# Kernel optimization log

Measured on AMD Instinct MI355X. Metric: run time of the kernel, lower is better.

## Reference

```python
import jax, jax.numpy as jnp
import numpy as np

RADIUS = 8.0   # matches init kwarg radius
EPS = 1e-8     # nn.CosineSimilarity eps


def _denorm(p, height, width):
    # kornia denormalize_pixel_coordinates: [-1,1] -> [0, size-1]
    scale = jnp.array([(width - 1) * 0.5, (height - 1) * 0.5], dtype=p.dtype)
    return (p + 1.0) * scale


def setup_inputs() -> dict:
    key = jax.random.key(0)
    k1, k2, k3, k4 = jax.random.split(key, 4)
    B, N, D = 4, 2048, 256
    features = jax.random.normal(k1, (B, N, D), dtype=jnp.float32)
    pts_src = jax.random.uniform(k2, (B, N, 2), dtype=jnp.float32) * 2.0 - 1.0
    pts_dst = jax.random.uniform(k3, (B, B, N, 2), dtype=jnp.float32) * 2.0 - 1.0
    invis_idx = jax.random.randint(k4, (3, 128), 0, N)
    return {"features": features, "pts_src": pts_src, "pts_dst": pts_dst,
            "invis_idx": invis_idx, "height": 480, "width": 640}


def reference(features, pts_src, pts_dst, invis_idx, height, width):
    # features: [B,N,D]; pts_src: [B,N,2]; pts_dst: [B,B,N,2]
    B, N, D = features.shape
    ps = _denorm(jax.lax.stop_gradient(pts_src), height, width)   # [B,N,2]
    pd = _denorm(jax.lax.stop_gradient(pts_dst), height, width)   # [B,B,N,2]

    # squared euclidean distance d2[i,j,n,m] = ||ps[i,n] - pd[i,j,m]||^2
    s_src = jnp.sum(ps * ps, axis=-1)          # [B,N]
    s_dst = jnp.sum(pd * pd, axis=-1)          # [B,B,N]
    cross = jnp.einsum('ind,ijmd->ijnm', ps, pd)
    d2 = s_src[:, None, :, None] + s_dst[:, :, None, :] - 2.0 * cross  # [B,B,N,N]
    mask = d2 <= RADIUS * RADIUS

    # pair p = i*B + j of the flattened [B^2] grid matches src batch j (p % B)
    # with dst batch i (p // B):
    # cos[i,j,n,m] = <features[j,n], features[i,m]> / max(|f_jn|*|f_im|, eps)
    dots = jnp.einsum('jnd,imd->ijnm', features, features)  # [B,B,N,N]
    norms = jnp.sqrt(jnp.sum(features * features, axis=-1))  # [B,N]
    denom = jnp.maximum(norms[None, :, :, None] * norms[:, None, None, :], EPS)
    cos = dots / denom

    cnt = jnp.maximum(jnp.sum(mask), 1).astype(features.dtype)
    return jnp.sum(jnp.where(mask, 1.0 - cos, 0.0)) / cnt
```

## Files before the change

### kernel.cpp

```cpp
#include <hip/hip_runtime.h>

#define BB 4
#define NN 2048
#define DD 256
#define TILE_N 32
#define NPW 8
#define NT (NN / TILE_N)
#define MLEN NN
#define MCH (MLEN / 128)
#define WQ_CAP 128
#define NBLK (BB * BB * NT)

__global__ __launch_bounds__(256, 4) void scan_kernel(const float* __restrict__ feat,
                                                      const float* __restrict__ pts_src,
                                                      const float* __restrict__ pts_dst,
                                                      const int* __restrict__ hptr,
                                                      const int* __restrict__ wptr,
                                                      float* __restrict__ psum,
                                                      unsigned int* __restrict__ pcnt) {
    __shared__ unsigned int wq[4][WQ_CAP];
    __shared__ unsigned int wqc[4];
    __shared__ float bsum[4];
    __shared__ unsigned int bcnt[4];

    const int xcd  = blockIdx.x & 7;
    const int slot = blockIdx.x >> 3;
    const int pair = xcd | ((slot >> 6) << 3);
    const int tile = slot & 63;
    const int i = pair >> 2;
    const int j = pair & 3;
    const float sx = ((float)(*wptr) - 1.0f) * 0.5f;
    const float sy = ((float)(*hptr) - 1.0f) * 0.5f;

    const int wave = threadIdx.x >> 6;
    const int lane = threadIdx.x & 63;
    if (lane == 0) wqc[wave] = 0u;

    const int nbase = tile * TILE_N + wave * NPW;
    float psx[NPW], psy[NPW];
#pragma unroll
    for (int k = 0; k < NPW; ++k) {
        psx[k] = fmaf(pts_src[(size_t)(i * NN + nbase + k) * 2 + 0], sx, sx);
        psy[k] = fmaf(pts_src[(size_t)(i * NN + nbase + k) * 2 + 1], sy, sy);
    }

    const float4* pd = (const float4*)(pts_dst + (size_t)pair * NN * 2);

    float4 q = pd[lane];
#pragma unroll 4
    for (int c = 0; c < MCH; ++c) {
        float4 qn;
        if (c + 1 < MCH) qn = pd[(c + 1) * 64 + lane];
        const float qx0 = fmaf(q.x, sx, sx), qy0 = fmaf(q.y, sy, sy);
        const float qx1 = fmaf(q.z, sx, sx), qy1 = fmaf(q.w, sy, sy);
        float mn = 1e30f;
#pragma unroll
        for (int k = 0; k < NPW; ++k) {
            const float ax = psx[k] - qx0, ay = psy[k] - qy0;
            const float bx = psx[k] - qx1, by = psy[k] - qy1;
            mn = fminf(mn, fminf(fmaf(ax, ax, ay * ay), fmaf(bx, bx, by * by)));
        }
        if (__ballot(mn <= 64.0f)) {
            const unsigned int m2 = (unsigned int)(c * 128 + 2 * lane);
#pragma unroll
            for (int k = 0; k < NPW; ++k) {
                const float ax = psx[k] - qx0, ay = psy[k] - qy0;
                const float bx = psx[k] - qx1, by = psy[k] - qy1;
                const float d0 = fmaf(ax, ax, ay * ay);
                const float d1 = fmaf(bx, bx, by * by);
                if (fminf(d0, d1) <= 64.0f) {
                    if (d0 <= 64.0f) {
                        const unsigned int slot2 = atomicAdd(&wqc[wave], 1u);
                        if (slot2 < WQ_CAP) wq[wave][slot2] = ((unsigned int)k << 11) | m2;
                    }
                    if (d1 <= 64.0f) {
                        const unsigned int slot2 = atomicAdd(&wqc[wave], 1u);
                        if (slot2 < WQ_CAP) wq[wave][slot2] = ((unsigned int)k << 11) | (m2 + 1u);
                    }
                }
            }
        }
        q = qn;
    }

    const unsigned int hc = min(wqc[wave], (unsigned int)WQ_CAP);
    const int g = lane >> 3, sub = lane & 7;
    float lsum = 0.0f;
    for (unsigned int h0 = 0; h0 < hc; h0 += 8) {
        const unsigned int hid = h0 + (unsigned int)g;
        const bool valid = hid < hc;
        float dd = 0.0f, aa = 0.0f, bb = 0.0f;
        if (valid) {
            const unsigned int rec = wq[wave][hid];
            const int m = (int)(rec & 2047u);
            const int n = nbase + (int)(rec >> 11);
            const float4* pa = (const float4*)(feat + (size_t)(j * NN + n) * DD);
            const float4* pb = (const float4*)(feat + (size_t)(i * NN + m) * DD);
#pragma unroll
            for (int t = 0; t < 8; ++t) {
                const float4 a = pa[t * 8 + sub];
                const float4 b = pb[t * 8 + sub];
                dd = fmaf(a.x, b.x, fmaf(a.y, b.y, fmaf(a.z, b.z, fmaf(a.w, b.w, dd))));
                aa = fmaf(a.x, a.x, fmaf(a.y, a.y, fmaf(a.z, a.z, fmaf(a.w, a.w, aa))));
                bb = fmaf(b.x, b.x, fmaf(b.y, b.y, fmaf(b.z, b.z, fmaf(b.w, b.w, bb))));
            }
        }
        dd += __shfl_xor(dd, 1, 64);  aa += __shfl_xor(aa, 1, 64);  bb += __shfl_xor(bb, 1, 64);
        dd += __shfl_xor(dd, 2, 64);  aa += __shfl_xor(aa, 2, 64);  bb += __shfl_xor(bb, 2, 64);
        dd += __shfl_xor(dd, 4, 64);  aa += __shfl_xor(aa, 4, 64);  bb += __shfl_xor(bb, 4, 64);
        if (valid && sub == 0) {
            const float p = aa * bb;
            float r = rsqrtf(p);
            r = r * (1.5f - 0.5f * p * r * r);
            lsum += 1.0f - dd * r;
        }
    }
#pragma unroll
    for (int off = 32; off >= 1; off >>= 1) lsum += __shfl_xor(lsum, off, 64);

    if (lane == 0) { bsum[wave] = lsum; bcnt[wave] = hc; }
    __syncthreads();
    if (threadIdx.x == 0) {
        psum[blockIdx.x] = bsum[0] + bsum[1] + bsum[2] + bsum[3];
        pcnt[blockIdx.x] = bcnt[0] + bcnt[1] + bcnt[2] + bcnt[3];
    }
}

__global__ __launch_bounds__(256) void finalize_kernel(const float* __restrict__ psum,
                                                       const unsigned int* __restrict__ pcnt,
                                                       float* __restrict__ out) {
    float s = 0.0f;
    float c = 0.0f;
    for (int t = threadIdx.x; t < NBLK; t += 256) {
        s += psum[t];
        c += (float)pcnt[t];
    }
#pragma unroll
    for (int off = 32; off >= 1; off >>= 1) {
        s += __shfl_xor(s, off, 64);
        c += __shfl_xor(c, off, 64);
    }
    __shared__ float ss[4], cc[4];
    const int wave = threadIdx.x >> 6;
    const int lane = threadIdx.x & 63;
    if (lane == 0) { ss[wave] = s; cc[wave] = c; }
    __syncthreads();
    if (threadIdx.x == 0) {
        const float S = ss[0] + ss[1] + ss[2] + ss[3];
        const float C = cc[0] + cc[1] + cc[2] + cc[3];
        out[0] = S / fmaxf(C, 1.0f);
    }
}

extern "C" void kernel_launch(void* const* d_in, const int* in_sizes, int n_in,
                              void* d_out, int out_size, void* d_ws, size_t ws_size,
                              hipStream_t stream) {
    const float* feat    = (const float*)d_in[0];
    const float* pts_src = (const float*)d_in[1];
    const float* pts_dst = (const float*)d_in[2];
    const int* hptr = (const int*)d_in[4];
    const int* wptr = (const int*)d_in[5];
    float* out = (float*)d_out;

    float*        psum  = (float*)d_ws;
    unsigned int* pcnt  = (unsigned int*)((char*)d_ws + 8192);

    scan_kernel<<<NBLK, 256, 0, stream>>>(feat, pts_src, pts_dst,
                                          hptr, wptr, psum, pcnt);
    finalize_kernel<<<1, 256, 0, stream>>>(psum, pcnt, out);
}
```

Baseline: 88.71 us.

## Fuse finalize into scan kernel via keyed per-block records and spin-wait

Removes the separate finalize kernel launch. Each block publishes its partial sum and count together with two block-specific key words using release stores. Block 0 spin-waits with acquire loads until every record shows its keys, then reduces and writes the output. This saves one kernel launch and its gap, but block 0 stays resident and busy-waits, and if it were scheduled before the others could run this could deadlock. The keys only guard against stale workspace contents by chance, since the workspace is never cleared between calls.

```diff
diff --git a/kernel.cpp b/kernel.cpp
--- a/kernel.cpp
+++ b/kernel.cpp
@@ -11,17 +11,21 @@
 #define WQ_CAP 128
 #define NBLK (BB * BB * NT)
 
+#define KEY1 0xA5C3E7D1u
+#define KEY2 0x3B9ACA07u
+
 __global__ __launch_bounds__(256, 4) void scan_kernel(const float* __restrict__ feat,
                                                       const float* __restrict__ pts_src,
                                                       const float* __restrict__ pts_dst,
                                                       const int* __restrict__ hptr,
                                                       const int* __restrict__ wptr,
-                                                      float* __restrict__ psum,
-                                                      unsigned int* __restrict__ pcnt) {
+                                                      unsigned int* __restrict__ recs,
+                                                      float* __restrict__ out) {
     __shared__ unsigned int wq[4][WQ_CAP];
     __shared__ unsigned int wqc[4];
     __shared__ float bsum[4];
     __shared__ unsigned int bcnt[4];
+    __shared__ float rsum[4], rcnt[4];
 
     const int xcd  = blockIdx.x & 7;
     const int slot = blockIdx.x >> 3;
@@ -70,12 +74,12 @@
                 const float d1 = fmaf(bx, bx, by * by);
                 if (fminf(d0, d1) <= 64.0f) {
                     if (d0 <= 64.0f) {
-                        const unsigned int slot2 = atomicAdd(&wqc[wave], 1u);
-                        if (slot2 < WQ_CAP) wq[wave][slot2] = ((unsigned int)k << 11) | m2;
+                        const unsigned int s2 = atomicAdd(&wqc[wave], 1u);
+                        if (s2 < WQ_CAP) wq[wave][s2] = ((unsigned int)k << 11) | m2;
                     }
                     if (d1 <= 64.0f) {
-                        const unsigned int slot2 = atomicAdd(&wqc[wave], 1u);
-                        if (slot2 < WQ_CAP) wq[wave][slot2] = ((unsigned int)k << 11) | (m2 + 1u);
+                        const unsigned int s2 = atomicAdd(&wqc[wave], 1u);
+                        if (s2 < WQ_CAP) wq[wave][s2] = ((unsigned int)k << 11) | (m2 + 1u);
                     }
                 }
             }
@@ -121,33 +125,39 @@
     if (lane == 0) { bsum[wave] = lsum; bcnt[wave] = hc; }
     __syncthreads();
     if (threadIdx.x == 0) {
-        psum[blockIdx.x] = bsum[0] + bsum[1] + bsum[2] + bsum[3];
-        pcnt[blockIdx.x] = bcnt[0] + bcnt[1] + bcnt[2] + bcnt[3];
+        const float S = bsum[0] + bsum[1] + bsum[2] + bsum[3];
+        const unsigned int C = bcnt[0] + bcnt[1] + bcnt[2] + bcnt[3];
+        unsigned int* rec = recs + 4u * blockIdx.x;
+        __hip_atomic_store(rec + 0, __float_as_uint(S), __ATOMIC_RELAXED, __HIP_MEMORY_SCOPE_AGENT);
+        __hip_atomic_store(rec + 1, C,                  __ATOMIC_RELAXED, __HIP_MEMORY_SCOPE_AGENT);
+        __hip_atomic_store(rec + 2, KEY1 ^ blockIdx.x,  __ATOMIC_RELEASE, __HIP_MEMORY_SCOPE_AGENT);
+        __hip_atomic_store(rec + 3, KEY2 ^ blockIdx.x,  __ATOMIC_RELEASE, __HIP_MEMORY_SCOPE_AGENT);
     }
-}
+    if (blockIdx.x != 0) return;
 
-__global__ __launch_bounds__(256) void finalize_kernel(const float* __restrict__ psum,
-                                                       const unsigned int* __restrict__ pcnt,
-                                                       float* __restrict__ out) {
-    float s = 0.0f;
-    float c = 0.0f;
+    float s = 0.0f, c = 0.0f;
     for (int t = threadIdx.x; t < NBLK; t += 256) {
-        s += psum[t];
-        c += (float)pcnt[t];
+        unsigned int* rec = recs + 4u * (unsigned int)t;
+        const unsigned int e1 = KEY1 ^ (unsigned int)t;
+        const unsigned int e2 = KEY2 ^ (unsigned int)t;
+        while (__hip_atomic_load(rec + 2, __ATOMIC_ACQUIRE, __HIP_MEMORY_SCOPE_AGENT) != e1 ||
+               __hip_atomic_load(rec + 3, __ATOMIC_ACQUIRE, __HIP_MEMORY_SCOPE_AGENT) != e2) {
+            __builtin_amdgcn_s_sleep(8);
+        }
+        s += __uint_as_float(__hip_atomic_load(rec + 0, __ATOMIC_RELAXED, __HIP_MEMORY_SCOPE_AGENT));
+        c += (float)__hip_atomic_load(rec + 1, __ATOMIC_RELAXED, __HIP_MEMORY_SCOPE_AGENT);
     }
 #pragma unroll
     for (int off = 32; off >= 1; off >>= 1) {
         s += __shfl_xor(s, off, 64);
         c += __shfl_xor(c, off, 64);
     }
-    __shared__ float ss[4], cc[4];
-    const int wave = threadIdx.x >> 6;
-    const int lane = threadIdx.x & 63;
-    if (lane == 0) { ss[wave] = s; cc[wave] = c; }
+    __syncthreads();
+    if (lane == 0) { rsum[wave] = s; rcnt[wave] = c; }
     __syncthreads();
     if (threadIdx.x == 0) {
-        const float S = ss[0] + ss[1] + ss[2] + ss[3];
-        const float C = cc[0] + cc[1] + cc[2] + cc[3];
+        const float S = rsum[0] + rsum[1] + rsum[2] + rsum[3];
+        const float C = rcnt[0] + rcnt[1] + rcnt[2] + rcnt[3];
         out[0] = S / fmaxf(C, 1.0f);
     }
 }
@@ -162,10 +172,8 @@
     const int* wptr = (const int*)d_in[5];
     float* out = (float*)d_out;
 
-    float*        psum  = (float*)d_ws;
-    unsigned int* pcnt  = (unsigned int*)((char*)d_ws + 8192);
+    unsigned int* recs = (unsigned int*)d_ws;
 
     scan_kernel<<<NBLK, 256, 0, stream>>>(feat, pts_src, pts_dst,
-                                          hptr, wptr, psum, pcnt);
-    finalize_kernel<<<1, 256, 0, stream>>>(psum, pcnt, out);
+                                          hptr, wptr, recs, out);
 }
```

Measured after the change: 110.9 us. +25.0%, slower.

## Replace brute-force radius scan with uniform spatial grid binning of dst points

Applied to the files above, without the earlier changes.

Adds a build kernel that buckets each pair's destination points into a 40x30 grid of 16-pixel cells using a counting sort with a shared prefix scan. The match kernel then checks only the 3x3 neighbouring cells for each source point, split across 8 column octants per tile, in place of scanning all 2048 dst points. This removes the O(N^2) distance work but adds an extra launch, serial per-thread loops of uneven length, and a gather through the permutation array. Each wave's hit queue is capped at 160 entries for 64 source points, so dense neighbourhoods could overflow and be silently dropped.

```diff
diff --git a/kernel.cpp b/kernel.cpp
--- a/kernel.cpp
+++ b/kernel.cpp
@@ -3,21 +3,103 @@
 #define BB 4
 #define NN 2048
 #define DD 256
-#define TILE_N 32
-#define NPW 8
-#define NT (NN / TILE_N)
-#define MLEN NN
-#define MCH (MLEN / 128)
-#define WQ_CAP 128
-#define NBLK (BB * BB * NT)
-
-__global__ __launch_bounds__(256, 4) void scan_kernel(const float* __restrict__ feat,
-                                                      const float* __restrict__ pts_src,
-                                                      const float* __restrict__ pts_dst,
-                                                      const int* __restrict__ hptr,
-                                                      const int* __restrict__ wptr,
-                                                      float* __restrict__ psum,
-                                                      unsigned int* __restrict__ pcnt) {
+#define GCX 40
+#define GCY 30
+#define NCELL (GCX * GCY)
+#define CSTRIDE 1216
+#define OCTW 5
+#define STILE 256
+#define NTIL (NN / STILE)
+#define MBLK (BB * BB * NTIL * 8)
+#define WQ_CAP 160
+
+#define OFF_BX    131072
+#define OFF_BM    (131072 + 262144)
+#define OFF_PSUM  (131072 + 262144 + 131072)
+#define OFF_PCNT  (OFF_PSUM + 4096)
+
+__device__ __forceinline__ int cell_clamp(int v, int hi) {
+    return v < 0 ? 0 : (v > hi ? hi : v);
+}
+
+__global__ __launch_bounds__(256) void build_kernel(const float* __restrict__ pts_dst,
+                                                    const int* __restrict__ hptr,
+                                                    const int* __restrict__ wptr,
+                                                    int* __restrict__ starts,
+                                                    float2* __restrict__ bx,
+                                                    int* __restrict__ bm) {
+    __shared__ int cnt[NCELL];
+    __shared__ int tsum[256];
+    const int pair = blockIdx.x;
+    const float sx = ((float)(*wptr) - 1.0f) * 0.5f;
+    const float sy = ((float)(*hptr) - 1.0f) * 0.5f;
+
+    for (int t = threadIdx.x; t < NCELL; t += 256) cnt[t] = 0;
+    __syncthreads();
+
+    const float2* pd = (const float2*)(pts_dst + (size_t)pair * NN * 2);
+    float qx[8], qy[8]; int qc[8];
+#pragma unroll
+    for (int k = 0; k < 8; ++k) {
+        const float2 r = pd[threadIdx.x + k * 256];
+        qx[k] = fmaf(r.x, sx, sx);
+        qy[k] = fmaf(r.y, sy, sy);
+        const int cx = cell_clamp((int)(qx[k] * 0.0625f), GCX - 1);
+        const int cy = cell_clamp((int)(qy[k] * 0.0625f), GCY - 1);
+        qc[k] = cx + GCX * cy;
+        atomicAdd(&cnt[qc[k]], 1);
+    }
+    __syncthreads();
+
+    const int base = threadIdx.x * 5;
+    int loc[5]; int s = 0;
+#pragma unroll
+    for (int k = 0; k < 5; ++k) {
+        const int c = base + k;
+        const int v = (c < NCELL) ? cnt[c] : 0;
+        loc[k] = s; s += v;
+    }
+    tsum[threadIdx.x] = s;
+    __syncthreads();
+    for (int off = 1; off < 256; off <<= 1) {
+        const int v = (threadIdx.x >= off) ? tsum[threadIdx.x - off] : 0;
+        __syncthreads();
+        tsum[threadIdx.x] += v;
+        __syncthreads();
+    }
+    const int tbase = tsum[threadIdx.x] - s;
+    int* gst = starts + pair * CSTRIDE;
+#pragma unroll
+    for (int k = 0; k < 5; ++k) {
+        const int c = base + k;
+        if (c < NCELL) {
+            const int st = tbase + loc[k];
+            gst[c] = st;
+            cnt[c] = st;
+        }
+    }
+    if (threadIdx.x == 0) gst[NCELL] = NN;
+    __syncthreads();
+
+    float2* gbx = bx + (size_t)pair * NN;
+    int*    gbm = bm + (size_t)pair * NN;
+#pragma unroll
+    for (int k = 0; k < 8; ++k) {
+        const int pos = atomicAdd(&cnt[qc[k]], 1);
+        gbx[pos] = make_float2(qx[k], qy[k]);
+        gbm[pos] = threadIdx.x + k * 256;
+    }
+}
+
+__global__ __launch_bounds__(256, 4) void match_kernel(const float* __restrict__ feat,
+                                                       const float* __restrict__ pts_src,
+                                                       const int* __restrict__ hptr,
+                                                       const int* __restrict__ wptr,
+                                                       const int* __restrict__ starts,
+                                                       const float2* __restrict__ bx,
+                                                       const int* __restrict__ bm,
+                                                       float* __restrict__ psum,
+                                                       unsigned int* __restrict__ pcnt) {
     __shared__ unsigned int wq[4][WQ_CAP];
     __shared__ unsigned int wqc[4];
     __shared__ float bsum[4];
@@ -25,8 +107,10 @@
 
     const int xcd  = blockIdx.x & 7;
     const int slot = blockIdx.x >> 3;
-    const int pair = xcd | ((slot >> 6) << 3);
-    const int tile = slot & 63;
+    const int pair = (xcd << 1) | (slot >> 6);
+    const int rest = slot & 63;
+    const int tile = rest >> 3;
+    const int oct  = rest & 7;
     const int i = pair >> 2;
     const int j = pair & 3;
     const float sx = ((float)(*wptr) - 1.0f) * 0.5f;
@@ -36,51 +120,36 @@
     const int lane = threadIdx.x & 63;
     if (lane == 0) wqc[wave] = 0u;
 
-    const int nbase = tile * TILE_N + wave * NPW;
-    float psx[NPW], psy[NPW];
-#pragma unroll
-    for (int k = 0; k < NPW; ++k) {
-        psx[k] = fmaf(pts_src[(size_t)(i * NN + nbase + k) * 2 + 0], sx, sx);
-        psy[k] = fmaf(pts_src[(size_t)(i * NN + nbase + k) * 2 + 1], sy, sy);
-    }
-
-    const float4* pd = (const float4*)(pts_dst + (size_t)pair * NN * 2);
-
-    float4 q = pd[lane];
-#pragma unroll 4
-    for (int c = 0; c < MCH; ++c) {
-        float4 qn;
-        if (c + 1 < MCH) qn = pd[(c + 1) * 64 + lane];
-        const float qx0 = fmaf(q.x, sx, sx), qy0 = fmaf(q.y, sy, sy);
-        const float qx1 = fmaf(q.z, sx, sx), qy1 = fmaf(q.w, sy, sy);
-        float mn = 1e30f;
-#pragma unroll
-        for (int k = 0; k < NPW; ++k) {
-            const float ax = psx[k] - qx0, ay = psy[k] - qy0;
-            const float bx = psx[k] - qx1, by = psy[k] - qy1;
-            mn = fminf(mn, fminf(fmaf(ax, ax, ay * ay), fmaf(bx, bx, by * by)));
-        }
-        if (__ballot(mn <= 64.0f)) {
-            const unsigned int m2 = (unsigned int)(c * 128 + 2 * lane);
-#pragma unroll
-            for (int k = 0; k < NPW; ++k) {
-                const float ax = psx[k] - qx0, ay = psy[k] - qy0;
-                const float bx = psx[k] - qx1, by = psy[k] - qy1;
-                const float d0 = fmaf(ax, ax, ay * ay);
-                const float d1 = fmaf(bx, bx, by * by);
-                if (fminf(d0, d1) <= 64.0f) {
-                    if (d0 <= 64.0f) {
-                        const unsigned int slot2 = atomicAdd(&wqc[wave], 1u);
-                        if (slot2 < WQ_CAP) wq[wave][slot2] = ((unsigned int)k << 11) | m2;
-                    }
-                    if (d1 <= 64.0f) {
-                        const unsigned int slot2 = atomicAdd(&wqc[wave], 1u);
-                        if (slot2 < WQ_CAP) wq[wave][slot2] = ((unsigned int)k << 11) | (m2 + 1u);
-                    }
+    const int nloc = threadIdx.x;
+    const float2 r = ((const float2*)pts_src)[(size_t)i * NN + tile * STILE + nloc];
+    const float px = fmaf(r.x, sx, sx);
+    const float py = fmaf(r.y, sy, sy);
+    const int cxs = cell_clamp((int)(px * 0.0625f), GCX - 1);
+    const int cys = cell_clamp((int)(py * 0.0625f), GCY - 1);
+
+    const int*    gst = starts + pair * CSTRIDE;
+    const float2* gbx = bx + (size_t)pair * NN;
+    const int*    gbm = bm + (size_t)pair * NN;
+
+#pragma unroll
+    for (int dy = -1; dy <= 1; ++dy) {
+        const int cy2 = cys + dy;
+        if ((unsigned)cy2 >= (unsigned)GCY) continue;
+#pragma unroll
+        for (int dx = -1; dx <= 1; ++dx) {
+            const int cx2 = cxs + dx;
+            if ((unsigned)(cx2 - oct * OCTW) >= (unsigned)OCTW) continue;
+            const int c = cx2 + GCX * cy2;
+            const int e = gst[c + 1];
+            for (int idx = gst[c]; idx < e; ++idx) {
+                const float2 q = gbx[idx];
+                const float ax = px - q.x, ay = py - q.y;
+                if (fmaf(ax, ax, ay * ay) <= 64.0f) {
+                    const unsigned int s2 = atomicAdd(&wqc[wave], 1u);
+                    if (s2 < WQ_CAP) wq[wave][s2] = ((unsigned int)nloc << 11) | (unsigned int)idx;
                 }
             }
         }
-        q = qn;
     }
 
     const unsigned int hc = min(wqc[wave], (unsigned int)WQ_CAP);
@@ -92,8 +161,8 @@
         float dd = 0.0f, aa = 0.0f, bb = 0.0f;
         if (valid) {
             const unsigned int rec = wq[wave][hid];
-            const int m = (int)(rec & 2047u);
-            const int n = nbase + (int)(rec >> 11);
+            const int m = gbm[rec & 2047u];
+            const int n = tile * STILE + (int)(rec >> 11);
             const float4* pa = (const float4*)(feat + (size_t)(j * NN + n) * DD);
             const float4* pb = (const float4*)(feat + (size_t)(i * NN + m) * DD);
 #pragma unroll
@@ -110,9 +179,9 @@
         dd += __shfl_xor(dd, 4, 64);  aa += __shfl_xor(aa, 4, 64);  bb += __shfl_xor(bb, 4, 64);
         if (valid && sub == 0) {
             const float p = aa * bb;
-            float r = rsqrtf(p);
-            r = r * (1.5f - 0.5f * p * r * r);
-            lsum += 1.0f - dd * r;
+            float rr = rsqrtf(p);
+            rr = rr * (1.5f - 0.5f * p * rr * rr);
+            lsum += 1.0f - dd * rr;
         }
     }
 #pragma unroll
@@ -131,7 +200,7 @@
                                                        float* __restrict__ out) {
     float s = 0.0f;
     float c = 0.0f;
-    for (int t = threadIdx.x; t < NBLK; t += 256) {
+    for (int t = threadIdx.x; t < MBLK; t += 256) {
         s += psum[t];
         c += (float)pcnt[t];
     }
@@ -162,10 +231,14 @@
     const int* wptr = (const int*)d_in[5];
     float* out = (float*)d_out;
 
-    float*        psum  = (float*)d_ws;
-    unsigned int* pcnt  = (unsigned int*)((char*)d_ws + 8192);
-
-    scan_kernel<<<NBLK, 256, 0, stream>>>(feat, pts_src, pts_dst,
-                                          hptr, wptr, psum, pcnt);
+    int*          starts = (int*)d_ws;
+    float2*       bx     = (float2*)((char*)d_ws + OFF_BX);
+    int*          bm     = (int*)((char*)d_ws + OFF_BM);
+    float*        psum   = (float*)((char*)d_ws + OFF_PSUM);
+    unsigned int* pcnt   = (unsigned int*)((char*)d_ws + OFF_PCNT);
+
+    build_kernel<<<BB * BB, 256, 0, stream>>>(pts_dst, hptr, wptr, starts, bx, bm);
+    match_kernel<<<MBLK, 256, 0, stream>>>(feat, pts_src, hptr, wptr,
+                                           starts, bx, bm, psum, pcnt);
     finalize_kernel<<<1, 256, 0, stream>>>(psum, pcnt, out);
 }
```

Result: slower. 93.71 us (+5.6%).
